# Kernel optimization log

Measured on AMD Instinct MI355X. Metric: run time of the kernel, lower is better.

Reference implementation:

```python
import jax, jax.numpy as jnp
import numpy as np

NB, D, ED, N, K, DTR = 4, 1024, 2048, 32, 4, 64
B, L = 1, 1024


def setup_inputs():
    key = jax.random.key(0)
    ks = jax.random.split(key, 10)
    g = lambda k, s, sc=0.02: jax.random.normal(k, s, dtype=jnp.float32) * sc
    A_log = jnp.log(jnp.broadcast_to(jnp.arange(1, N + 1, dtype=jnp.float32), (NB, ED, N))) + 0.0
    return {
        "x": g(ks[0], (B, L, D), 1.0),
        "Wi": g(ks[1], (D, D)),
        "bi": jnp.zeros((D,), jnp.float32),
        "ln_g": jnp.ones((NB, D), jnp.float32),
        "ln_b": jnp.zeros((NB, D), jnp.float32),
        "in_w": g(ks[2], (NB, 2 * ED, D)),
        "conv_w": g(ks[3], (NB, ED, 1, K), 0.2),
        "conv_b": jnp.zeros((NB, ED), jnp.float32),
        "xproj_w": g(ks[4], (NB, DTR + 2 * N, ED)),
        "dtproj_w": g(ks[5], (NB, ED, DTR), 0.1),
        "dtproj_b": jnp.full((NB, ED), -4.0, jnp.float32),
        "A_log": A_log,
        "Dp": jnp.ones((NB, ED), jnp.float32),
        "out_w": g(ks[6], (NB, D, ED)),
        "fn_g": jnp.ones((D,), jnp.float32),
        "fn_b": jnp.zeros((D,), jnp.float32),
        "sp_w": g(ks[7], (N, D)),
        "sp_b": jnp.zeros((N,), jnp.float32),
    }


def layernorm(x, g, b, eps=1e-5):
    m = jnp.mean(x, axis=-1, keepdims=True)
    v = jnp.mean(jnp.square(x - m), axis=-1, keepdims=True)
    return (x - m) * jax.lax.rsqrt(v + eps) * g + b


def mamba(u_in, in_w, conv_w, conv_b, xproj_w, dtproj_w, dtproj_b, A_log, Dp, out_w):
    # u_in: (B, L, D)
    xz = u_in @ in_w.T                       # (B, L, 2*ED)
    u, z = jnp.split(xz, 2, axis=-1)         # each (B, L, ED)
    # causal depthwise conv over time
    uc = jnp.swapaxes(u, 1, 2)               # (B, ED, L)
    uc = jax.lax.conv_general_dilated(uc, conv_w, (1,), [(K - 1, 0)], feature_group_count=ED)
    uc = uc + conv_b[None, :, None]
    u = jax.nn.silu(jnp.swapaxes(uc, 1, 2))  # (B, L, ED)
    x_dbl = u @ xproj_w.T                    # (B, L, DTR + 2N)
    dt, Bm, Cm = jnp.split(x_dbl, [DTR, DTR + N], axis=-1)
    delta = jax.nn.softplus(dt @ dtproj_w.T + dtproj_b)  # (B, L, ED)
    A = -jnp.exp(A_log)                                  # (ED, N)
    dA = jnp.exp(delta[..., None] * A)                   # (B, L, ED, N)
    dBu = (delta * u)[..., None] * Bm[:, :, None, :]     # (B, L, ED, N)

    def step(h, inp):
        dA_t, dBu_t, C_t = inp
        h = dA_t * h + dBu_t
        y = jnp.einsum('ben,bn->be', h, C_t)
        return h, y

    h0 = jnp.zeros((u.shape[0], ED, N), u.dtype)
    _, ys = jax.lax.scan(step, h0, (jnp.swapaxes(dA, 0, 1), jnp.swapaxes(dBu, 0, 1), jnp.swapaxes(Cm, 0, 1)))
    y = jnp.swapaxes(ys, 0, 1) + u * Dp      # (B, L, ED)
    y = y * jax.nn.silu(z)
    return y @ out_w.T                       # (B, L, D)


def reference(x, Wi, bi, ln_g, ln_b, in_w, conv_w, conv_b, xproj_w, dtproj_w, dtproj_b, A_log, Dp, out_w, fn_g, fn_b, sp_w, sp_b):
    h = x @ Wi.T + bi
    for i in range(NB):
        normed = layernorm(h, ln_g[i], ln_b[i])
        h = h + mamba(normed, in_w[i], conv_w[i], conv_b[i], xproj_w[i],
                      dtproj_w[i], dtproj_b[i], A_log[i], Dp[i], out_w[i])
    h = layernorm(h, fn_g, fn_b)
    state = jnp.mean(h, axis=1) @ sp_w.T + sp_b   # (B, N)
    return h, state
```

## Files before the change

kernel.cpp:

```cpp
#include <hip/hip_runtime.h>
#include <math.h>

#define D_    1024
#define ED_   2048
#define NST   32
#define KCONV 4
#define DTR_  64
#define L_    1024
#define NB_   4
#define NCH   8
#define CHUNK (L_ / NCH)
#define ZSPL  4
#define XPZ   16

typedef __bf16 bf16_8 __attribute__((ext_vector_type(8)));
typedef __bf16 bf16_4 __attribute__((ext_vector_type(4)));
typedef float  f32x4  __attribute__((ext_vector_type(4)));

__device__ __forceinline__ float softplus_f(float x) {
  return x > 20.f ? x : log1pf(expf(x));
}
__device__ __forceinline__ float silu_f(float x) {
  return x / (1.f + expf(-x));
}

__device__ __forceinline__ int xcd_swz(int lin, int nwg) {
  const int q = nwg >> 3;
  return (lin & 7) * q + (lin >> 3);
}

__global__ __launch_bounds__(256) void f2bf4_k(
    const float* __restrict__ i0, __bf16* __restrict__ o0, int n0,
    const float* __restrict__ i1, __bf16* __restrict__ o1, int n1,
    const float* __restrict__ i2, __bf16* __restrict__ o2, int n2,
    const float* __restrict__ i3, __bf16* __restrict__ o3, int n3)
{
  int gid = blockIdx.x * 256 + threadIdx.x;
  const int u0 = n0 >> 3, u1 = n1 >> 3, u2 = n2 >> 3, u3 = n3 >> 3;
  const float* in; __bf16* out;
  if (gid < u0) { in = i0; out = o0; }
  else if ((gid -= u0) < u1) { in = i1; out = o1; }
  else if ((gid -= u1) < u2) { in = i2; out = o2; }
  else if ((gid -= u2) < u3) { in = i3; out = o3; }
  else return;
  const int i = gid * 8;
  const float4 a = *reinterpret_cast<const float4*>(in + i);
  const float4 b = *reinterpret_cast<const float4*>(in + i + 4);
  bf16_8 v;
  v[0]=(__bf16)a.x; v[1]=(__bf16)a.y; v[2]=(__bf16)a.z; v[3]=(__bf16)a.w;
  v[4]=(__bf16)b.x; v[5]=(__bf16)b.y; v[6]=(__bf16)b.z; v[7]=(__bf16)b.w;
  *reinterpret_cast<bf16_8*>(out + i) = v;
}

__global__ __launch_bounds__(256) void gemm_mfma(
    const __bf16* __restrict__ A, int lda,
    const __bf16* __restrict__ W, int ldw,
    const float* __restrict__ bias, float* __restrict__ C, int ldc,
    int K, int flags)
{
  __shared__ __bf16 As[128 * 64];
  __shared__ __bf16 Ws[128 * 64];
  const int tid  = threadIdx.x;
  const int lane = tid & 63;
  const int w    = tid >> 6;
  const int wr   = w >> 1, wc = w & 1;
  const int nwg  = gridDim.x * gridDim.y;
  const int swz  = xcd_swz(blockIdx.y * gridDim.x + blockIdx.x, nwg);
  const int bx   = swz % gridDim.x, by = swz / gridDim.x;
  const int row0 = by * 128, col0 = bx * 128;

  f32x4 acc[4][4] = {};

  for (int k0 = 0; k0 < K; k0 += 64) {
    #pragma unroll
    for (int j = 0; j < 4; ++j) {
      const int inst = w * 4 + j;
      const int row  = inst * 8 + (lane >> 3);
      const int lu   = (lane & 7) ^ (row & 7);
      __builtin_amdgcn_global_load_lds(
          (const __attribute__((address_space(1))) void*)(A + (size_t)(row0 + row) * lda + k0 + lu * 8),
          (__attribute__((address_space(3))) void*)(&As[inst * 512]), 16, 0, 0);
      __builtin_amdgcn_global_load_lds(
          (const __attribute__((address_space(1))) void*)(W + (size_t)(col0 + row) * ldw + k0 + lu * 8),
          (__attribute__((address_space(3))) void*)(&Ws[inst * 512]), 16, 0, 0);
    }
    __syncthreads();
    const int r16 = lane & 15;
    const int uq  = lane >> 4;
    #pragma unroll
    for (int ks = 0; ks < 2; ++ks) {
      bf16_8 af[4], bfr[4];
      #pragma unroll
      for (int m = 0; m < 4; ++m) {
        const int row = wr * 64 + m * 16 + r16;
        const int pu  = (ks * 4 + uq) ^ (row & 7);
        af[m] = *reinterpret_cast<const bf16_8*>(&As[row * 64 + pu * 8]);
      }
      #pragma unroll
      for (int n = 0; n < 4; ++n) {
        const int row = wc * 64 + n * 16 + r16;
        const int pu  = (ks * 4 + uq) ^ (row & 7);
        bfr[n] = *reinterpret_cast<const bf16_8*>(&Ws[row * 64 + pu * 8]);
      }
      #pragma unroll
      for (int m = 0; m < 4; ++m)
        #pragma unroll
        for (int n = 0; n < 4; ++n)
          acc[m][n] = __builtin_amdgcn_mfma_f32_16x16x32_bf16(af[m], bfr[n], acc[m][n], 0, 0, 0);
    }
    __syncthreads();
  }

  const int crow = (lane >> 4) * 4;
  const int ccol = lane & 15;
  #pragma unroll
  for (int m = 0; m < 4; ++m)
    #pragma unroll
    for (int n = 0; n < 4; ++n) {
      const int col = col0 + wc * 64 + n * 16 + ccol;
      const float bv = (flags & 4) ? bias[col] : 0.f;
      #pragma unroll
      for (int r = 0; r < 4; ++r) {
        const int row = row0 + wr * 64 + m * 16 + crow + r;
        float* cp = C + (size_t)row * ldc + col;
        float v = acc[m][n][r] + bv;
        if (flags & 2) v = softplus_f(v);
        if (flags & 1) v += *cp;
        *cp = v;
      }
    }
}

__global__ __launch_bounds__(256) void gemm_mfma_sk(
    const __bf16* __restrict__ A, const __bf16* __restrict__ W,
    float* __restrict__ partials, int M, int N, int K, int Kc)
{
  __shared__ __bf16 As[128 * 64];
  __shared__ __bf16 Ws[128 * 64];
  const int tid  = threadIdx.x;
  const int lane = tid & 63;
  const int w    = tid >> 6;
  const int wr   = w >> 1, wc = w & 1;
  const int nwg  = gridDim.x * gridDim.y * gridDim.z;
  const int lin  = (blockIdx.z * gridDim.y + blockIdx.y) * gridDim.x + blockIdx.x;
  const int swz  = xcd_swz(lin, nwg);
  const int bx   = swz % gridDim.x;
  const int tmp  = swz / gridDim.x;
  const int by   = tmp % gridDim.y, bz = tmp / gridDim.y;
  const int row0 = by * 128, col0 = bx * 128;
  const int kbase = bz * Kc;

  f32x4 acc[4][4] = {};

  for (int k0 = kbase; k0 < kbase + Kc; k0 += 64) {
    #pragma unroll
    for (int j = 0; j < 4; ++j) {
      const int inst = w * 4 + j;
      const int row  = inst * 8 + (lane >> 3);
      const int lu   = (lane & 7) ^ (row & 7);
      __builtin_amdgcn_global_load_lds(
          (const __attribute__((address_space(1))) void*)(A + (size_t)(row0 + row) * K + k0 + lu * 8),
          (__attribute__((address_space(3))) void*)(&As[inst * 512]), 16, 0, 0);
      __builtin_amdgcn_global_load_lds(
          (const __attribute__((address_space(1))) void*)(W + (size_t)(col0 + row) * K + k0 + lu * 8),
          (__attribute__((address_space(3))) void*)(&Ws[inst * 512]), 16, 0, 0);
    }
    __syncthreads();
    const int r16 = lane & 15;
    const int uq  = lane >> 4;
    #pragma unroll
    for (int ks = 0; ks < 2; ++ks) {
      bf16_8 af[4], bfr[4];
      #pragma unroll
      for (int m = 0; m < 4; ++m) {
        const int row = wr * 64 + m * 16 + r16;
        const int pu  = (ks * 4 + uq) ^ (row & 7);
        af[m] = *reinterpret_cast<const bf16_8*>(&As[row * 64 + pu * 8]);
      }
      #pragma unroll
      for (int n = 0; n < 4; ++n) {
        const int row = wc * 64 + n * 16 + r16;
        const int pu  = (ks * 4 + uq) ^ (row & 7);
        bfr[n] = *reinterpret_cast<const bf16_8*>(&Ws[row * 64 + pu * 8]);
      }
      #pragma unroll
      for (int m = 0; m < 4; ++m)
        #pragma unroll
        for (int n = 0; n < 4; ++n)
          acc[m][n] = __builtin_amdgcn_mfma_f32_16x16x32_bf16(af[m], bfr[n], acc[m][n], 0, 0, 0);
    }
    __syncthreads();
  }

  float* base = partials + (size_t)bz * M * N;
  const int crow = (lane >> 4) * 4;
  const int ccol = lane & 15;
  #pragma unroll
  for (int m = 0; m < 4; ++m)
    #pragma unroll
    for (int n = 0; n < 4; ++n) {
      const int col = col0 + wc * 64 + n * 16 + ccol;
      #pragma unroll
      for (int r = 0; r < 4; ++r) {
        const int row = row0 + wr * 64 + m * 16 + crow + r;
        base[(size_t)row * N + col] = acc[m][n][r];
      }
    }
}

__global__ __launch_bounds__(256) void mfma_sk_reduce(
    const float* __restrict__ partials, const float* __restrict__ bias,
    float* __restrict__ C, __bf16* __restrict__ Cbf,
    int elems, int ncols, int nz, int flags)
{
  const int i = (blockIdx.x * 256 + threadIdx.x) * 4;
  if (i >= elems) return;
  float4 s = *reinterpret_cast<const float4*>(partials + i);
  for (int z = 1; z < nz; ++z) {
    const float4 p = *reinterpret_cast<const float4*>(partials + (size_t)z * elems + i);
    s.x += p.x; s.y += p.y; s.z += p.z; s.w += p.w;
  }
  if (flags & 4) {
    const float4 bv = *reinterpret_cast<const float4*>(bias + (i % ncols));
    s.x += bv.x; s.y += bv.y; s.z += bv.z; s.w += bv.w;
  }
  if (flags & 1) {
    const float4 ov = *reinterpret_cast<const float4*>(C + i);
    s.x += ov.x; s.y += ov.y; s.z += ov.z; s.w += ov.w;
  }
  *reinterpret_cast<float4*>(C + i) = s;
  if (flags & 8) {
    bf16_4 b;
    b[0]=(__bf16)s.x; b[1]=(__bf16)s.y; b[2]=(__bf16)s.z; b[3]=(__bf16)s.w;
    *reinterpret_cast<bf16_4*>(Cbf + i) = b;
  }
}

__global__ __launch_bounds__(256) void layernorm_k(
    const float* __restrict__ x, const float* __restrict__ g,
    const float* __restrict__ b, float* __restrict__ out)
{
  __shared__ float red[8];
  const int row = blockIdx.x;
  const int tid = threadIdx.x;
  const float* xr = x + (size_t)row * D_;
  float4 v = *reinterpret_cast<const float4*>(xr + tid * 4);
  float s = v.x + v.y + v.z + v.w;
  #pragma unroll
  for (int off = 32; off; off >>= 1) s += __shfl_down(s, off, 64);
  if ((tid & 63) == 0) red[tid >> 6] = s;
  __syncthreads();
  const float m = (red[0] + red[1] + red[2] + red[3]) * (1.f / D_);
  float dx0 = v.x - m, dx1 = v.y - m, dx2 = v.z - m, dx3 = v.w - m;
  float ss = dx0*dx0 + dx1*dx1 + dx2*dx2 + dx3*dx3;
  #pragma unroll
  for (int off = 32; off; off >>= 1) ss += __shfl_down(ss, off, 64);
  if ((tid & 63) == 0) red[4 + (tid >> 6)] = ss;
  __syncthreads();
  const float var = (red[4] + red[5] + red[6] + red[7]) * (1.f / D_);
  const float rs = rsqrtf(var + 1e-5f);
  const int c = tid * 4;
  const float4 gv = *reinterpret_cast<const float4*>(g + c);
  const float4 bv = *reinterpret_cast<const float4*>(b + c);
  float4 o;
  o.x = dx0 * rs * gv.x + bv.x;
  o.y = dx1 * rs * gv.y + bv.y;
  o.z = dx2 * rs * gv.z + bv.z;
  o.w = dx3 * rs * gv.w + bv.w;
  *reinterpret_cast<float4*>(out + (size_t)row * D_ + c) = o;
}

__global__ __launch_bounds__(256) void layernorm_bf_k(
    const float* __restrict__ x, const float* __restrict__ g,
    const float* __restrict__ b, __bf16* __restrict__ out)
{
  __shared__ float red[8];
  const int row = blockIdx.x;
  const int tid = threadIdx.x;
  const float* xr = x + (size_t)row * D_;
  float4 v = *reinterpret_cast<const float4*>(xr + tid * 4);
  float s = v.x + v.y + v.z + v.w;
  #pragma unroll
  for (int off = 32; off; off >>= 1) s += __shfl_down(s, off, 64);
  if ((tid & 63) == 0) red[tid >> 6] = s;
  __syncthreads();
  const float m = (red[0] + red[1] + red[2] + red[3]) * (1.f / D_);
  float dx0 = v.x - m, dx1 = v.y - m, dx2 = v.z - m, dx3 = v.w - m;
  float ss = dx0*dx0 + dx1*dx1 + dx2*dx2 + dx3*dx3;
  #pragma unroll
  for (int off = 32; off; off >>= 1) ss += __shfl_down(ss, off, 64);
  if ((tid & 63) == 0) red[4 + (tid >> 6)] = ss;
  __syncthreads();
  const float var = (red[4] + red[5] + red[6] + red[7]) * (1.f / D_);
  const float rs = rsqrtf(var + 1e-5f);
  const int c = tid * 4;
  const float4 gv = *reinterpret_cast<const float4*>(g + c);
  const float4 bv = *reinterpret_cast<const float4*>(b + c);
  bf16_4 o;
  o[0] = (__bf16)(dx0 * rs * gv.x + bv.x);
  o[1] = (__bf16)(dx1 * rs * gv.y + bv.y);
  o[2] = (__bf16)(dx2 * rs * gv.z + bv.z);
  o[3] = (__bf16)(dx3 * rs * gv.w + bv.w);
  *reinterpret_cast<bf16_4*>(out + (size_t)row * D_ + c) = o;
}

__global__ __launch_bounds__(256) void conv_silu_k(
    const float* __restrict__ xz, const float* __restrict__ cw,
    const float* __restrict__ cb, float* __restrict__ u, __bf16* __restrict__ ub)
{
  const int e = blockIdx.x * 256 + threadIdx.x;
  const int t0 = blockIdx.y * 8;
  const float w0 = cw[e*4+0], w1 = cw[e*4+1], w2 = cw[e*4+2], w3 = cw[e*4+3];
  const float b = cb[e];
  float x0 = (t0 >= 3) ? xz[(size_t)(t0-3)*(2*ED_)+e] : 0.f;
  float x1 = (t0 >= 2) ? xz[(size_t)(t0-2)*(2*ED_)+e] : 0.f;
  float x2 = (t0 >= 1) ? xz[(size_t)(t0-1)*(2*ED_)+e] : 0.f;
  #pragma unroll
  for (int j = 0; j < 8; ++j) {
    const float x3 = xz[(size_t)(t0+j)*(2*ED_)+e];
    const float uv = silu_f(b + w0*x0 + w1*x1 + w2*x2 + w3*x3);
    u[(size_t)(t0+j)*ED_+e] = uv;
    ub[(size_t)(t0+j)*ED_+e] = (__bf16)uv;
    x0 = x1; x1 = x2; x2 = x3;
  }
}

__global__ __launch_bounds__(256) void scan_phase1(
    const float* __restrict__ delta, const float* __restrict__ u,
    const float* __restrict__ xdbl, const float* __restrict__ A_log,
    float* __restrict__ hend, float* __restrict__ Pend)
{
  __shared__ float dl[16][8], ul[16][8];
  __shared__ float bl[16][32];
  const int tid = threadIdx.x;
  const int n = tid & 31;
  const int c = tid >> 5;
  const int e0 = blockIdx.x * 8;
  const int e = e0 + c;
  const int ch = blockIdx.y;
  const float a = -expf(A_log[e * NST + n]);
  float h = 0.f, S = 0.f;
  const int t0 = ch * CHUNK;
  const int s_t = (tid & 127) >> 3, s_e = tid & 7;
  const int b_c = (tid & 7) * 4;

  float rg_a = 0.f;
  float4 rg_b;
  if (tid < 128) {
    rg_a = delta[(size_t)(t0 + s_t) * ED_ + e0 + s_e];
    rg_b = *reinterpret_cast<const float4*>(&xdbl[(size_t)(t0 + s_t) * 128 + 64 + b_c]);
  } else {
    rg_a = u[(size_t)(t0 + s_t) * ED_ + e0 + s_e];
  }

  for (int tb = 0; tb < CHUNK; tb += 16) {
    if (tid < 128) {
      dl[s_t][s_e] = rg_a;
      *reinterpret_cast<float4*>(&bl[s_t][b_c]) = rg_b;
    } else {
      ul[s_t][s_e] = rg_a;
    }
    __syncthreads();
    if (tb + 16 < CHUNK) {
      const int t = t0 + tb + 16 + s_t;
      if (tid < 128) {
        rg_a = delta[(size_t)t * ED_ + e0 + s_e];
        rg_b = *reinterpret_cast<const float4*>(&xdbl[(size_t)t * 128 + 64 + b_c]);
      } else {
        rg_a = u[(size_t)t * ED_ + e0 + s_e];
      }
    }
    #pragma unroll
    for (int j = 0; j < 16; ++j) {
      const float sd = dl[j][c];
      const float uv = ul[j][c];
      const float Bv = bl[j][n];
      h = fmaf(__expf(sd * a), h, sd * uv * Bv);
      S += sd;
    }
    __syncthreads();
  }
  const int idx = ch * (ED_ * NST) + blockIdx.x * 256 + tid;
  hend[idx] = h;
  Pend[idx] = __expf(a * S);
}

__global__ __launch_bounds__(256, 7) void scan_phase3(
    const float* __restrict__ delta, const float* __restrict__ u,
    const float* __restrict__ xdbl, const float* __restrict__ A_log,
    const float* __restrict__ hend, const float* __restrict__ Pend,
    const float* __restrict__ Dp,
    const float* __restrict__ xz, __bf16* __restrict__ y)
{
  __shared__ float p_lds[8][16][33];
  __shared__ float dl[16][8], ul[16][8], zl[16][8];
  __shared__ float bc[16][64];
  const int tid = threadIdx.x;
  const int n = tid & 31;
  const int c = tid >> 5;
  const int e0 = blockIdx.x * 8;
  const int e = e0 + c;
  const int ch = blockIdx.y;
  const float a = -expf(A_log[e * NST + n]);
  const float dp = Dp[e];

  float h = 0.f;
  {
    const int sidx = blockIdx.x * 256 + tid;
    for (int cc = 0; cc < ch; ++cc) {
      const int off = cc * (ED_ * NST) + sidx;
      h = fmaf(Pend[off], h, hend[off]);
    }
  }

  const int t0 = ch * CHUNK;
  const int r = n & 15, half = n >> 4;
  const int s_t  = (tid & 127) >> 3;
  const int s_e  = tid & 7;
  const int b_t  = tid >> 4;
  const int b_c  = (tid & 15) * 4;

  float rg_a = 0.f, rg_z = 0.f;
  float4 rg_bc;
  {
    const int t = t0 + s_t;
    if (tid < 128) {
      rg_a = delta[(size_t)t * ED_ + e0 + s_e];
      rg_z = xz[(size_t)t * (2*ED_) + ED_ + e0 + s_e];
    } else {
      rg_a = u[(size_t)t * ED_ + e0 + s_e];
    }
    rg_bc = *reinterpret_cast<const float4*>(&xdbl[(size_t)(t0 + b_t) * 128 + 64 + b_c]);
  }

  for (int tb = 0; tb < CHUNK; tb += 16) {
    if (tid < 128) { dl[s_t][s_e] = rg_a; zl[s_t][s_e] = rg_z; }
    else          { ul[s_t][s_e] = rg_a; }
    *reinterpret_cast<float4*>(&bc[b_t][b_c]) = rg_bc;
    __syncthreads();
    if (tb + 16 < CHUNK) {
      const int t = t0 + tb + 16 + s_t;
      if (tid < 128) {
        rg_a = delta[(size_t)t * ED_ + e0 + s_e];
        rg_z = xz[(size_t)t * (2*ED_) + ED_ + e0 + s_e];
      } else {
        rg_a = u[(size_t)t * ED_ + e0 + s_e];
      }
      rg_bc = *reinterpret_cast<const float4*>(&xdbl[(size_t)(t0 + tb + 16 + b_t) * 128 + 64 + b_c]);
    }
    #pragma unroll
    for (int j = 0; j < 16; ++j) {
      const float sd = dl[j][c];
      const float uv = ul[j][c];
      const float Bv = bc[j][n];
      const float Cv = bc[j][32 + n];
      const float dA = __expf(sd * a);
      h = fmaf(dA, h, sd * uv * Bv);
      p_lds[c][j][n] = h * Cv;
    }
    __syncthreads();
    float s = 0.f;
    #pragma unroll
    for (int k = 0; k < 16; ++k) s += p_lds[c][r][half * 16 + k];
    s += __shfl_xor(s, 16, 64);
    if (half == 0) {
      const float uvt = ul[r][c];
      const float zv  = zl[r][c];
      y[(size_t)(t0 + tb + r) * ED_ + e] = (__bf16)((s + uvt * dp) * silu_f(zv));
    }
    __syncthreads();
  }
}

__global__ __launch_bounds__(256) void colmean_part_k(
    const float* __restrict__ hf, float* __restrict__ part)
{
  const int d = blockIdx.x * 256 + threadIdx.x;
  const int tc = blockIdx.y;
  float s = 0.f;
  #pragma unroll 8
  for (int j = 0; j < 32; ++j) s += hf[(size_t)(tc * 32 + j) * D_ + d];
  part[tc * D_ + d] = s;
}

__global__ __launch_bounds__(256) void state_fused_k(
    const float* __restrict__ part, const float* __restrict__ spw,
    const float* __restrict__ spb, float* __restrict__ out)
{
  __shared__ float red[4];
  const int nidx = blockIdx.x;
  const int tid = threadIdx.x;
  float s = 0.f;
  for (int d = tid; d < D_; d += 256) {
    float cm = 0.f;
    #pragma unroll
    for (int c = 0; c < 32; ++c) cm += part[c * D_ + d];
    s += cm * (1.f / L_) * spw[(size_t)nidx * D_ + d];
  }
  #pragma unroll
  for (int off = 32; off; off >>= 1) s += __shfl_down(s, off, 64);
  if ((tid & 63) == 0) red[tid >> 6] = s;
  __syncthreads();
  if (tid == 0) out[nidx] = red[0] + red[1] + red[2] + red[3] + spb[nidx];
}

extern "C" void kernel_launch(void* const* d_in, const int* in_sizes, int n_in,
                              void* d_out, int out_size, void* d_ws, size_t ws_size,
                              hipStream_t stream) {
  const float* x        = (const float*)d_in[0];
  const float* Wi       = (const float*)d_in[1];
  const float* bi       = (const float*)d_in[2];
  const float* ln_g     = (const float*)d_in[3];
  const float* ln_b     = (const float*)d_in[4];
  const float* in_w     = (const float*)d_in[5];
  const float* conv_w   = (const float*)d_in[6];
  const float* conv_b   = (const float*)d_in[7];
  const float* xproj_w  = (const float*)d_in[8];
  const float* dtproj_w = (const float*)d_in[9];
  const float* dtproj_b = (const float*)d_in[10];
  const float* A_log    = (const float*)d_in[11];
  const float* Dp       = (const float*)d_in[12];
  const float* out_w    = (const float*)d_in[13];
  const float* fn_g     = (const float*)d_in[14];
  const float* fn_b     = (const float*)d_in[15];
  const float* sp_w     = (const float*)d_in[16];
  const float* sp_b     = (const float*)d_in[17];
  float* out  = (float*)d_out;
  float* ws_f = (float*)d_ws;

  float* h_buf  = ws_f;
  float* xz     = ws_f + 1048576;
  float* u_buf  = ws_f + 5242880;
  float* xdbl   = ws_f + 7340032;
  float* delta  = ws_f + 7471104;
  float* hend   = ws_f + 9568256;
  float* pend   = ws_f + 10092544;
  __bf16* nbf   = (__bf16*)(ws_f + 10617856);
  __bf16* ybf   = (__bf16*)(ws_f + 11142144);
  __bf16* wbf   = (__bf16*)(ws_f + 12190720);
  __bf16* xdblbf= (__bf16*)(ws_f + 16385024);
  __bf16* dtwbf = (__bf16*)(ws_f + 16450560);
  __bf16* ubf   = (__bf16*)(ws_f + 16516096);
  __bf16* xpbf  = (__bf16*)(ws_f + 17564672);
  __bf16* owbf  = (__bf16*)(ws_f + 17695744);
  float* skmf   = u_buf;
  float* skxp   = delta;
  float* cmpart = hend;

  const dim3 blk(256);

  f2bf4_k<<<1024, blk, 0, stream>>>(x, nbf, L_*D_, Wi, wbf, D_*D_,
                                    x, nbf, 0, x, nbf, 0);
  gemm_mfma_sk<<<dim3(D_/128, L_/128, ZSPL), blk, 0, stream>>>(
      nbf, wbf, skmf, L_, D_, D_, D_/ZSPL);
  mfma_sk_reduce<<<dim3(L_*D_/4/256), blk, 0, stream>>>(
      skmf, bi, h_buf, nullptr, L_*D_, D_, ZSPL, 4);

  for (int i = 0; i < NB_; ++i) {
    f2bf4_k<<<3264, blk, 0, stream>>>(
        in_w    + (size_t)i*2*ED_*D_, wbf,   2*ED_*D_,
        xproj_w + (size_t)i*128*ED_,  xpbf,  128*ED_,
        dtproj_w+ (size_t)i*ED_*DTR_, dtwbf, ED_*DTR_,
        out_w   + (size_t)i*D_*ED_,   owbf,  D_*ED_);
    layernorm_bf_k<<<L_, blk, 0, stream>>>(h_buf, ln_g + i*D_, ln_b + i*D_, nbf);
    gemm_mfma<<<dim3(2*ED_/128, L_/128), blk, 0, stream>>>(
        nbf, D_, wbf, D_, nullptr, xz, 2*ED_, D_, 0);
    conv_silu_k<<<dim3(ED_/256, L_/8), blk, 0, stream>>>(
        xz, conv_w + (size_t)i*ED_*KCONV, conv_b + (size_t)i*ED_, u_buf, ubf);
    gemm_mfma_sk<<<dim3(1, L_/128, XPZ), blk, 0, stream>>>(
        ubf, xpbf, skxp, L_, 128, ED_, ED_/XPZ);
    mfma_sk_reduce<<<dim3(L_*128/4/256), blk, 0, stream>>>(
        skxp, nullptr, xdbl, xdblbf, L_*128, 128, XPZ, 8);
    gemm_mfma<<<dim3(ED_/128, L_/128), blk, 0, stream>>>(
        xdblbf, 128, dtwbf, DTR_, dtproj_b + (size_t)i*ED_, delta, ED_, DTR_, 2 | 4);
    scan_phase1<<<dim3(ED_/8, NCH), blk, 0, stream>>>(
        delta, u_buf, xdbl, A_log + (size_t)i*ED_*NST, hend, pend);
    scan_phase3<<<dim3(ED_/8, NCH), blk, 0, stream>>>(
        delta, u_buf, xdbl, A_log + (size_t)i*ED_*NST, hend, pend,
        Dp + (size_t)i*ED_, xz, ybf);
    gemm_mfma_sk<<<dim3(D_/128, L_/128, ZSPL), blk, 0, stream>>>(
        ybf, owbf, skmf, L_, D_, ED_, ED_/ZSPL);
    mfma_sk_reduce<<<dim3(L_*D_/4/256), blk, 0, stream>>>(
        skmf, nullptr, h_buf, nullptr, L_*D_, D_, ZSPL, 1);
  }

  layernorm_k<<<L_, blk, 0, stream>>>(h_buf, fn_g, fn_b, out);
  colmean_part_k<<<dim3(D_/256, 32), blk, 0, stream>>>(out, cmpart);
  state_fused_k<<<NST, blk, 0, stream>>>(cmpart, sp_w, sp_b, out + (size_t)L_*D_);
}
```

Measured before the change: 650.4 us.

## Widen scan blocks to 16 channels with 512 threads

Both scan kernels now process 16 ED channels per block with 512 threads instead of 8 channels with 256. Each block's B/C tile is shared by twice as many channels, which halves redundant xdbl loads and the number of blocks. Staging loads are redistributed so the lower half loads delta/z and the upper half loads u plus B/C. The grid shrinks to 1024 blocks, which lowers parallelism slack, and the occupancy hint of 7 on phase3 is dropped while its LDS use per block doubles.

```diff
diff --git a/kernel.cpp b/kernel.cpp
--- a/kernel.cpp
+++ b/kernel.cpp
@@ -325,49 +325,52 @@
   }
 }
 
-__global__ __launch_bounds__(256) void scan_phase1(
+__global__ __launch_bounds__(512) void scan_phase1(
     const float* __restrict__ delta, const float* __restrict__ u,
     const float* __restrict__ xdbl, const float* __restrict__ A_log,
     float* __restrict__ hend, float* __restrict__ Pend)
 {
-  __shared__ float dl[16][8], ul[16][8];
-  __shared__ float bl[16][32];
+  __shared__ float dl[16][16], ul[16][16];
+  __shared__ float bl[16][36];
   const int tid = threadIdx.x;
   const int n = tid & 31;
   const int c = tid >> 5;
-  const int e0 = blockIdx.x * 8;
+  const int e0 = blockIdx.x * 16;
   const int e = e0 + c;
   const int ch = blockIdx.y;
   const float a = -expf(A_log[e * NST + n]);
   float h = 0.f, S = 0.f;
   const int t0 = ch * CHUNK;
-  const int s_t = (tid & 127) >> 3, s_e = tid & 7;
-  const int b_c = (tid & 7) * 4;
+  const int s_t = (tid & 255) >> 4, s_e = tid & 15;
+  const int bidx = tid - 256;
+  const int b_t = bidx >> 3, b_c = (bidx & 7) * 4;
 
   float rg_a = 0.f;
   float4 rg_b;
-  if (tid < 128) {
+  if (tid < 256) {
     rg_a = delta[(size_t)(t0 + s_t) * ED_ + e0 + s_e];
-    rg_b = *reinterpret_cast<const float4*>(&xdbl[(size_t)(t0 + s_t) * 128 + 64 + b_c]);
   } else {
     rg_a = u[(size_t)(t0 + s_t) * ED_ + e0 + s_e];
+    if (bidx < 128)
+      rg_b = *reinterpret_cast<const float4*>(&xdbl[(size_t)(t0 + b_t) * 128 + 64 + b_c]);
   }
 
   for (int tb = 0; tb < CHUNK; tb += 16) {
-    if (tid < 128) {
+    if (tid < 256) {
       dl[s_t][s_e] = rg_a;
-      *reinterpret_cast<float4*>(&bl[s_t][b_c]) = rg_b;
     } else {
       ul[s_t][s_e] = rg_a;
+      if (bidx < 128) *reinterpret_cast<float4*>(&bl[b_t][b_c]) = rg_b;
     }
     __syncthreads();
     if (tb + 16 < CHUNK) {
       const int t = t0 + tb + 16 + s_t;
-      if (tid < 128) {
+      if (tid < 256) {
         rg_a = delta[(size_t)t * ED_ + e0 + s_e];
-        rg_b = *reinterpret_cast<const float4*>(&xdbl[(size_t)t * 128 + 64 + b_c]);
       } else {
         rg_a = u[(size_t)t * ED_ + e0 + s_e];
+        if (bidx < 128)
+          rg_b = *reinterpret_cast<const float4*>(&xdbl[(size_t)(t0 + tb + 16 + b_t) * 128 + 64 + b_c]);
       }
     }
     #pragma unroll
@@ -380,25 +383,25 @@
     }
     __syncthreads();
   }
-  const int idx = ch * (ED_ * NST) + blockIdx.x * 256 + tid;
+  const int idx = ch * (ED_ * NST) + blockIdx.x * 512 + tid;
   hend[idx] = h;
   Pend[idx] = __expf(a * S);
 }
 
-__global__ __launch_bounds__(256, 7) void scan_phase3(
+__global__ __launch_bounds__(512) void scan_phase3(
     const float* __restrict__ delta, const float* __restrict__ u,
     const float* __restrict__ xdbl, const float* __restrict__ A_log,
     const float* __restrict__ hend, const float* __restrict__ Pend,
     const float* __restrict__ Dp,
     const float* __restrict__ xz, __bf16* __restrict__ y)
 {
-  __shared__ float p_lds[8][16][33];
-  __shared__ float dl[16][8], ul[16][8], zl[16][8];
-  __shared__ float bc[16][64];
+  __shared__ float p_lds[16][16][33];
+  __shared__ float dl[16][16], ul[16][16], zl[16][16];
+  __shared__ float bc[16][68];
   const int tid = threadIdx.x;
   const int n = tid & 31;
   const int c = tid >> 5;
-  const int e0 = blockIdx.x * 8;
+  const int e0 = blockIdx.x * 16;
   const int e = e0 + c;
   const int ch = blockIdx.y;
   const float a = -expf(A_log[e * NST + n]);
@@ -406,7 +409,7 @@
 
   float h = 0.f;
   {
-    const int sidx = blockIdx.x * 256 + tid;
+    const int sidx = blockIdx.x * 512 + tid;
     for (int cc = 0; cc < ch; ++cc) {
       const int off = cc * (ED_ * NST) + sidx;
       h = fmaf(Pend[off], h, hend[off]);
@@ -415,38 +418,42 @@
 
   const int t0 = ch * CHUNK;
   const int r = n & 15, half = n >> 4;
-  const int s_t  = (tid & 127) >> 3;
-  const int s_e  = tid & 7;
-  const int b_t  = tid >> 4;
-  const int b_c  = (tid & 15) * 4;
+  const int s_t  = (tid & 255) >> 4;
+  const int s_e  = tid & 15;
+  const int bidx = tid - 256;
+  const int b_t  = (bidx & 255) >> 4;
+  const int b_c  = (bidx & 15) * 4;
 
   float rg_a = 0.f, rg_z = 0.f;
   float4 rg_bc;
   {
     const int t = t0 + s_t;
-    if (tid < 128) {
+    if (tid < 256) {
       rg_a = delta[(size_t)t * ED_ + e0 + s_e];
       rg_z = xz[(size_t)t * (2*ED_) + ED_ + e0 + s_e];
     } else {
       rg_a = u[(size_t)t * ED_ + e0 + s_e];
-    }
-    rg_bc = *reinterpret_cast<const float4*>(&xdbl[(size_t)(t0 + b_t) * 128 + 64 + b_c]);
+      rg_bc = *reinterpret_cast<const float4*>(&xdbl[(size_t)(t0 + b_t) * 128 + 64 + b_c]);
+    }
   }
 
   for (int tb = 0; tb < CHUNK; tb += 16) {
-    if (tid < 128) { dl[s_t][s_e] = rg_a; zl[s_t][s_e] = rg_z; }
-    else          { ul[s_t][s_e] = rg_a; }
-    *reinterpret_cast<float4*>(&bc[b_t][b_c]) = rg_bc;
+    if (tid < 256) {
+      dl[s_t][s_e] = rg_a; zl[s_t][s_e] = rg_z;
+    } else {
+      ul[s_t][s_e] = rg_a;
+      *reinterpret_cast<float4*>(&bc[b_t][b_c]) = rg_bc;
+    }
     __syncthreads();
     if (tb + 16 < CHUNK) {
       const int t = t0 + tb + 16 + s_t;
-      if (tid < 128) {
+      if (tid < 256) {
         rg_a = delta[(size_t)t * ED_ + e0 + s_e];
         rg_z = xz[(size_t)t * (2*ED_) + ED_ + e0 + s_e];
       } else {
         rg_a = u[(size_t)t * ED_ + e0 + s_e];
-      }
-      rg_bc = *reinterpret_cast<const float4*>(&xdbl[(size_t)(t0 + tb + 16 + b_t) * 128 + 64 + b_c]);
+        rg_bc = *reinterpret_cast<const float4*>(&xdbl[(size_t)(t0 + tb + 16 + b_t) * 128 + 64 + b_c]);
+      }
     }
     #pragma unroll
     for (int j = 0; j < 16; ++j) {
@@ -548,6 +555,7 @@
   float* cmpart = hend;
 
   const dim3 blk(256);
+  const dim3 blk512(512);
 
   f2bf4_k<<<1024, blk, 0, stream>>>(x, nbf, L_*D_, Wi, wbf, D_*D_,
                                     x, nbf, 0, x, nbf, 0);
@@ -573,9 +581,9 @@
         skxp, nullptr, xdbl, xdblbf, L_*128, 128, XPZ, 8);
     gemm_mfma<<<dim3(ED_/128, L_/128), blk, 0, stream>>>(
         xdblbf, 128, dtwbf, DTR_, dtproj_b + (size_t)i*ED_, delta, ED_, DTR_, 2 | 4);
-    scan_phase1<<<dim3(ED_/8, NCH), blk, 0, stream>>>(
+    scan_phase1<<<dim3(ED_/16, NCH), blk512, 0, stream>>>(
         delta, u_buf, xdbl, A_log + (size_t)i*ED_*NST, hend, pend);
-    scan_phase3<<<dim3(ED_/8, NCH), blk, 0, stream>>>(
+    scan_phase3<<<dim3(ED_/16, NCH), blk512, 0, stream>>>(
         delta, u_buf, xdbl, A_log + (size_t)i*ED_*NST, hend, pend,
         Dp + (size_t)i*ED_, xz, ybf);
     gemm_mfma_sk<<<dim3(D_/128, L_/128, ZSPL), blk, 0, stream>>>(
```

After: 661.5 us. No clear change (+1.7%).
